# Optimization experiments

Hardware: AMD Instinct MI355X
Metric: run time of the kernel (lower is better)

The kernel has to match this reference:

```python
import jax, jax.numpy as jnp
import numpy as np

N_POINTS = 262144
SP_FEAT = 128
HIDDEN = 64
EMBED = 256
NUM_SP = 4096
NUM_SP2 = 256
PAD_LIMIT = 64
MASK_RATIO = 0.6


def setup_inputs() -> dict:
    key = jax.random.key(0)
    ks = jax.random.split(key, 6)
    x = jax.random.normal(ks[0], (N_POINTS, SP_FEAT), jnp.float32)
    # point -> superpoint ids, sorted; force every superpoint non-empty
    idx10 = jax.random.randint(ks[1], (N_POINTS,), 0, NUM_SP)
    idx10 = jnp.sort(idx10.at[:NUM_SP].set(jnp.arange(NUM_SP))).astype(jnp.int32)
    # superpoint -> higher superpoint, balanced (16 per group, < PAD_LIMIT), sorted
    idx21 = ((jnp.arange(NUM_SP) * NUM_SP2) // NUM_SP).astype(jnp.int32)
    # deterministic mask: exactly int(NUM_SP * MASK_RATIO) superpoints masked
    mask_num = int(NUM_SP * MASK_RATIO)
    perm = jax.random.permutation(ks[2], NUM_SP)
    is_masked = jnp.zeros((NUM_SP,), bool).at[perm[:mask_num]].set(True)
    W1 = jax.random.normal(ks[3], (SP_FEAT, HIDDEN), jnp.float32) / np.sqrt(SP_FEAT).astype(np.float32)
    b1 = jnp.zeros((HIDDEN,), jnp.float32)
    W2 = jax.random.normal(ks[4], (HIDDEN, EMBED), jnp.float32) / np.sqrt(HIDDEN).astype(np.float32)
    b2 = jnp.zeros((EMBED,), jnp.float32)
    return {
        "full_features": x,
        "full_super_indices_10": idx10,
        "full_super_indices_21": idx21,
        "is_masked": is_masked,
        "W1": W1, "b1": b1, "W2": W2, "b2": b2,
    }


def _pad_scatter(tokens, idx21, flag):
    # tokens: [NUM_SP, C]; idx21 sorted sp->sp2 ids; flag: [NUM_SP] bool.
    # rank of each flagged superpoint within its sp2 group (in sp order)
    f = flag.astype(jnp.int32)
    cum = jnp.cumsum(f)                                            # inclusive global cumsum
    per_group = jax.ops.segment_sum(f, idx21, num_segments=NUM_SP2)
    prefix = jnp.concatenate([jnp.zeros((1,), jnp.int32), jnp.cumsum(per_group)[:-1]])
    rank = cum - 1 - prefix[idx21]                                 # 0-based slot within group
    slot = jnp.where(flag, rank, PAD_LIMIT)                        # PAD_LIMIT -> dropped
    out = jnp.zeros((NUM_SP2, PAD_LIMIT, tokens.shape[-1]), tokens.dtype)
    return out.at[idx21, slot].set(tokens, mode="drop")


def reference(full_features, full_super_indices_10, full_super_indices_21,
              is_masked, W1, b1, W2, b2):
    # per-point 2-layer MLP (gather is implicit: MLP is pointwise), then segment max
    h = jax.nn.relu(full_features @ W1 + b1)                       # [N, HIDDEN]
    h = jax.nn.relu(h @ W2 + b2)                                   # [N, EMBED]
    tok = jax.ops.segment_max(h, full_super_indices_10, num_segments=NUM_SP)  # [NUM_SP, EMBED]
    remain_tokens = _pad_scatter(tok, full_super_indices_21, ~is_masked)      # [NUM_SP2, PAD, EMBED]
    mask_tokens = _pad_scatter(tok, full_super_indices_21, is_masked)         # [NUM_SP2, PAD, EMBED]
    return (remain_tokens, mask_tokens)
```

## Files before the change

kernel.cpp:

```cpp
#include <hip/hip_runtime.h>
#include <hip/hip_bf16.h>

#define N_POINTS 262144
#define SP_FEAT 128
#define HIDDEN 64
#define EMBED 256
#define NUM_SP 4096
#define NUM_SP2 256
#define PAD_LIMIT 64
#define SLOTS 4
#define OS_STRIDE 260
#define H1_STRIDE 76

typedef __bf16 bf16x8 __attribute__((ext_vector_type(8)));
typedef float floatx4 __attribute__((ext_vector_type(4)));
using bf16 = __hip_bfloat16;

__global__ __launch_bounds__(256) void fused_prep_kernel(
    const float* __restrict__ W1, const float* __restrict__ W2,
    const int* __restrict__ idx10, const int* __restrict__ idx21,
    const void* __restrict__ is_masked,
    bf16* __restrict__ W1t, bf16* __restrict__ W2t,
    int* __restrict__ start, int* __restrict__ invR, int* __restrict__ invM,
    float4* __restrict__ partial4)
{
    const int tid = threadIdx.x;
    const int blk = blockIdx.x;

    if (blk < 1024) {
        int z = blk * 256 + tid;
        float4 zv = {0.f, 0.f, 0.f, 0.f};
#pragma unroll
        for (int j = 0; j < 4; ++j)
            partial4[z + j * (1024 * 256)] = zv;
        return;
    }
    const int blk2 = blk - 1024;
    if (blk2 < 113) {
        int i = blk2 * 256 + tid;
        if (i < HIDDEN * SP_FEAT) {
            int n = i >> 7, k = i & 127;
            W1t[i] = __float2bfloat16(W1[k * HIDDEN + n]);
        } else if (i < HIDDEN * SP_FEAT + EMBED * HIDDEN) {
            int j = i - HIDDEN * SP_FEAT;
            int n = j >> 6, k = j & 63;
            W2t[j] = __float2bfloat16(W2[k * EMBED + n]);
        } else if (i <= HIDDEN * SP_FEAT + EMBED * HIDDEN + NUM_SP) {
            int s = i - (HIDDEN * SP_FEAT + EMBED * HIDDEN);
            if (s == NUM_SP) { start[s] = N_POINTS; return; }
            int a = 0, b = N_POINTS;
            while (a < b) { int m = (a + b) >> 1; if (idx10[m] < s) a = m + 1; else b = m; }
            start[s] = a;
        }
        return;
    }
    __shared__ int encS;
    if (tid == 0) encS = 0;
    __syncthreads();
    const unsigned char* mb = (const unsigned char*)is_masked;
    const int* mi = (const int*)is_masked;
    int local = 0;
    for (int p = tid; p < NUM_SP; p += 256)
        if ((p & 3) && mb[p]) local = 1;
    if (local) atomicOr(&encS, 1);
    __syncthreads();
    const int e = encS;

    const int g = tid;
    int a = 0, b = NUM_SP;
    while (a < b) { int m = (a + b) >> 1; if (idx21[m] < g) a = m + 1; else b = m; }
    int lo = a;
    b = NUM_SP;
    while (a < b) { int m = (a + b) >> 1; if (idx21[m] < g + 1) a = m + 1; else b = m; }
    int hi = a;
    int nR = 0, nM = 0;
    for (int s = lo; s < hi; ++s) {
        int msk = e ? (int)mb[s] : mi[s];
        if (msk) { if (nM < PAD_LIMIT) invM[g * PAD_LIMIT + nM] = s; nM++; }
        else     { if (nR < PAD_LIMIT) invR[g * PAD_LIMIT + nR] = s; nR++; }
    }
    for (int r = nR; r < PAD_LIMIT; ++r) invR[g * PAD_LIMIT + r] = -1;
    for (int r = nM; r < PAD_LIMIT; ++r) invM[g * PAD_LIMIT + r] = -1;
}

__global__ __launch_bounds__(256, 4) void mlp_segmax_kernel(
    const float* __restrict__ X, const int* __restrict__ idx10,
    const int* __restrict__ start,
    const bf16* __restrict__ W1t, const float* __restrict__ b1,
    const bf16* __restrict__ W2t, const float* __restrict__ b2,
    float* __restrict__ partial)
{
    __shared__ __align__(16) char smemU[64 * OS_STRIDE * 2];
    __shared__ int sIdx[64];
    bf16 (*Xs)[136]       = (bf16(*)[136])smemU;
    bf16 (*H1s)[H1_STRIDE] = (bf16(*)[H1_STRIDE])(smemU + 64 * 136 * 2);
    bf16 (*Os)[OS_STRIDE]  = (bf16(*)[OS_STRIDE])smemU;

    const int tid  = threadIdx.x;
    const int lane = tid & 63;
    const int w    = tid >> 6;
    const int l15  = lane & 15;
    const int quad = lane >> 4;
    const int b    = blockIdx.x;
    const int m0   = b * 64;

    bf16x8 bw1[4];
    {
        const bf16* p = W1t + (16 * w + l15) * SP_FEAT + quad * 8;
#pragma unroll
        for (int ks = 0; ks < 4; ++ks) bw1[ks] = *(const bf16x8*)(p + 32 * ks);
    }
    bf16x8 bf2[4][2];
#pragma unroll
    for (int tn = 0; tn < 4; ++tn) {
        const bf16* p = W2t + (64 * w + 16 * tn + l15) * HIDDEN + quad * 8;
#pragma unroll
        for (int ks = 0; ks < 2; ++ks) bf2[tn][ks] = *(const bf16x8*)(p + 32 * ks);
    }
    float b2f[4];
#pragma unroll
    for (int tn = 0; tn < 4; ++tn) b2f[tn] = b2[64 * w + 16 * tn + l15];
    const float b1v = b1[16 * w + l15];

#pragma unroll
    for (int i = 0; i < 4; ++i) {
        int c   = tid + 256 * i;
        int row = c >> 4;
        int cc  = (c & 15) * 8;
        const float* src = X + (size_t)(m0 + row) * SP_FEAT + cc;
        float4 u0 = *(const float4*)src;
        float4 u1 = *(const float4*)(src + 4);
        union { bf16x8 v; bf16 h[8]; } u;
        u.h[0] = __float2bfloat16(u0.x); u.h[1] = __float2bfloat16(u0.y);
        u.h[2] = __float2bfloat16(u0.z); u.h[3] = __float2bfloat16(u0.w);
        u.h[4] = __float2bfloat16(u1.x); u.h[5] = __float2bfloat16(u1.y);
        u.h[6] = __float2bfloat16(u1.z); u.h[7] = __float2bfloat16(u1.w);
        *(bf16x8*)(&Xs[row][cc]) = u.v;
    }
    if (tid < 64) sIdx[tid] = idx10[m0 + tid];
    __syncthreads();

    floatx4 zero4 = {0.f, 0.f, 0.f, 0.f};
    floatx4 acc1[4] = {zero4, zero4, zero4, zero4};
#pragma unroll
    for (int ks = 0; ks < 4; ++ks) {
        int k = ks * 32 + quad * 8;
#pragma unroll
        for (int tm = 0; tm < 4; ++tm) {
            bf16x8 a = *(bf16x8*)(&Xs[16 * tm + l15][k]);
            acc1[tm] = __builtin_amdgcn_mfma_f32_16x16x32_bf16(a, bw1[ks], acc1[tm], 0, 0, 0);
        }
    }
#pragma unroll
    for (int tm = 0; tm < 4; ++tm) {
#pragma unroll
        for (int r = 0; r < 4; ++r) {
            float v = acc1[tm][r] + b1v;
            v = v > 0.f ? v : 0.f;
            H1s[16 * tm + quad * 4 + r][16 * w + l15] = __float2bfloat16(v);
        }
    }
    __syncthreads();

    bf16x8 afr[4][2];
#pragma unroll
    for (int tm = 0; tm < 4; ++tm) {
        afr[tm][0] = *(bf16x8*)(&H1s[16 * tm + l15][quad * 8]);
        afr[tm][1] = *(bf16x8*)(&H1s[16 * tm + l15][32 + quad * 8]);
    }
    __syncthreads();

#pragma unroll
    for (int tm = 0; tm < 4; ++tm) {
#pragma unroll
        for (int tn = 0; tn < 4; ++tn) {
            floatx4 acc = zero4;
            acc = __builtin_amdgcn_mfma_f32_16x16x32_bf16(afr[tm][0], bf2[tn][0], acc, 0, 0, 0);
            acc = __builtin_amdgcn_mfma_f32_16x16x32_bf16(afr[tm][1], bf2[tn][1], acc, 0, 0, 0);
#pragma unroll
            for (int r = 0; r < 4; ++r) {
                float v = acc[r] + b2f[tn];
                v = v > 0.f ? v : 0.f;
                Os[16 * tm + quad * 4 + r][64 * w + 16 * tn + l15] = __float2bfloat16(v);
            }
        }
    }
    __syncthreads();

    {
        int cur_sp = sIdx[0];
        float cur  = __bfloat162float(Os[0][tid]);
        for (int r = 1; r < 64; ++r) {
            int sp = sIdx[r];
            float v = __bfloat162float(Os[r][tid]);
            if (sp != cur_sp) {
                int slot = b - (start[cur_sp] >> 6);
                int* dst = (int*)(partial + ((size_t)cur_sp * SLOTS + (slot < 3 ? slot : 3)) * EMBED + tid);
                if (slot < 3) *(float*)dst = cur;
                else atomicMax(dst, __float_as_int(cur));
                cur_sp = sp;
                cur = v;
            } else {
                cur = fmaxf(cur, v);
            }
        }
        int slot = b - (start[cur_sp] >> 6);
        int* dst = (int*)(partial + ((size_t)cur_sp * SLOTS + (slot < 3 ? slot : 3)) * EMBED + tid);
        if (slot < 3) *(float*)dst = cur;
        else atomicMax(dst, __float_as_int(cur));
    }
}

__global__ __launch_bounds__(256) void scatter_kernel(
    const float4* __restrict__ partial4, const int* __restrict__ invR,
    const int* __restrict__ invM, float4* __restrict__ out4)
{
    const int bb   = blockIdx.x;
    const int g    = bb & (NUM_SP2 - 1);
    const int slab = bb >> 8;
    const int tid  = threadIdx.x;
    const int c4   = tid & 63;
    const int r0   = tid >> 6;
    const int* tab = slab ? invM : invR;
    float4* o = out4 + ((size_t)slab * NUM_SP2 + g) * PAD_LIMIT * 64;
#pragma unroll 4
    for (int rr = 0; rr < 16; ++rr) {
        int row = r0 + rr * 4;
        int sp = tab[g * PAD_LIMIT + row];
        float4 v = {0.f, 0.f, 0.f, 0.f};
        if (sp >= 0) {
            const float4* p = partial4 + (size_t)sp * SLOTS * 64 + c4;
            float4 a = p[0], bq = p[64], c = p[128], d = p[192];
            v.x = fmaxf(fmaxf(a.x, bq.x), fmaxf(c.x, d.x));
            v.y = fmaxf(fmaxf(a.y, bq.y), fmaxf(c.y, d.y));
            v.z = fmaxf(fmaxf(a.z, bq.z), fmaxf(c.z, d.z));
            v.w = fmaxf(fmaxf(a.w, bq.w), fmaxf(c.w, d.w));
        }
        o[row * 64 + c4] = v;
    }
}

extern "C" void kernel_launch(void* const* d_in, const int* in_sizes, int n_in,
                              void* d_out, int out_size, void* d_ws, size_t ws_size,
                              hipStream_t stream) {
    (void)in_sizes; (void)n_in; (void)ws_size; (void)out_size;
    const float* X        = (const float*)d_in[0];
    const int* idx10      = (const int*)d_in[1];
    const int* idx21      = (const int*)d_in[2];
    const void* is_masked = (const void*)d_in[3];
    const float* W1       = (const float*)d_in[4];
    const float* b1       = (const float*)d_in[5];
    const float* W2       = (const float*)d_in[6];
    const float* b2       = (const float*)d_in[7];

    char* ws       = (char*)d_ws;
    float* partial = (float*)ws;
    bf16* W1t      = (bf16*)(ws + (size_t)NUM_SP * SLOTS * EMBED * 4);
    bf16* W2t      = W1t + HIDDEN * SP_FEAT;
    int*  start    = (int*)((char*)(W2t + EMBED * HIDDEN));
    int*  invR     = start + (NUM_SP + 2);
    int*  invM     = invR + NUM_SP2 * PAD_LIMIT;

    fused_prep_kernel<<<1138, 256, 0, stream>>>(
        W1, W2, idx10, idx21, is_masked, W1t, W2t, start, invR, invM,
        (float4*)partial);
    mlp_segmax_kernel<<<N_POINTS / 64, 256, 0, stream>>>(
        X, idx10, start, W1t, b1, W2t, b2, partial);
    scatter_kernel<<<NUM_SP2 * 2, 256, 0, stream>>>(
        (const float4*)partial, invR, invM, (float4*)d_out);
}
```

Before: 263.1 us.

## Fuse segment-max into MFMA epilogue, drop partial zeroing and binary-search start

The per-superpoint start offsets are now found by scanning for boundaries between neighbouring sorted indices instead of a binary search per superpoint. The 16 MB zero-fill of the partial buffer is removed. The second-layer MFMA epilogue now does the running segment max directly in registers and merges results through shared-memory atomics, replacing the bf16 output staging and its barriers. The scatter kernel reads only the partial slots a superpoint actually wrote. The risk is that atomicMax on slot 3 and on non-local superpoints now targets a partial buffer that was never initialised, which could give wrong results when a segment spans many blocks.

```diff
diff --git a/kernel.cpp b/kernel.cpp
--- a/kernel.cpp
+++ b/kernel.cpp
@@ -9,8 +9,9 @@
 #define NUM_SP2 256
 #define PAD_LIMIT 64
 #define SLOTS 4
-#define OS_STRIDE 260
+#define XS_STRIDE 136
 #define H1_STRIDE 76
+#define LOCAL_SP 8
 
 typedef __bf16 bf16x8 __attribute__((ext_vector_type(8)));
 typedef float floatx4 __attribute__((ext_vector_type(4)));
@@ -21,36 +22,33 @@
     const int* __restrict__ idx10, const int* __restrict__ idx21,
     const void* __restrict__ is_masked,
     bf16* __restrict__ W1t, bf16* __restrict__ W2t,
-    int* __restrict__ start, int* __restrict__ invR, int* __restrict__ invM,
-    float4* __restrict__ partial4)
+    int* __restrict__ start, int* __restrict__ invR, int* __restrict__ invM)
 {
     const int tid = threadIdx.x;
     const int blk = blockIdx.x;
 
-    if (blk < 1024) {
-        int z = blk * 256 + tid;
-        float4 zv = {0.f, 0.f, 0.f, 0.f};
-#pragma unroll
-        for (int j = 0; j < 4; ++j)
-            partial4[z + j * (1024 * 256)] = zv;
+    if (blk < 256) {
+        int p0 = (blk * 256 + tid) * 4;
+        int4 v = *(const int4*)(idx10 + p0);
+        if (p0 == 0) { start[0] = 0; start[NUM_SP] = N_POINTS; }
+        if (v.y != v.x) start[v.y] = p0 + 1;
+        if (v.z != v.y) start[v.z] = p0 + 2;
+        if (v.w != v.z) start[v.w] = p0 + 3;
+        if (p0 + 4 < N_POINTS) {
+            int nx = idx10[p0 + 4];
+            if (nx != v.w) start[nx] = p0 + 4;
+        }
         return;
     }
-    const int blk2 = blk - 1024;
-    if (blk2 < 113) {
-        int i = blk2 * 256 + tid;
+    if (blk < 352) {
+        int i = (blk - 256) * 256 + tid;
         if (i < HIDDEN * SP_FEAT) {
             int n = i >> 7, k = i & 127;
             W1t[i] = __float2bfloat16(W1[k * HIDDEN + n]);
-        } else if (i < HIDDEN * SP_FEAT + EMBED * HIDDEN) {
+        } else {
             int j = i - HIDDEN * SP_FEAT;
             int n = j >> 6, k = j & 63;
             W2t[j] = __float2bfloat16(W2[k * EMBED + n]);
-        } else if (i <= HIDDEN * SP_FEAT + EMBED * HIDDEN + NUM_SP) {
-            int s = i - (HIDDEN * SP_FEAT + EMBED * HIDDEN);
-            if (s == NUM_SP) { start[s] = N_POINTS; return; }
-            int a = 0, b = N_POINTS;
-            while (a < b) { int m = (a + b) >> 1; if (idx10[m] < s) a = m + 1; else b = m; }
-            start[s] = a;
         }
         return;
     }
@@ -90,11 +88,10 @@
     const bf16* __restrict__ W2t, const float* __restrict__ b2,
     float* __restrict__ partial)
 {
-    __shared__ __align__(16) char smemU[64 * OS_STRIDE * 2];
+    __shared__ __align__(16) bf16 Xs[64][XS_STRIDE];
+    __shared__ __align__(16) bf16 H1s[64][H1_STRIDE];
+    __shared__ int tokL[LOCAL_SP][EMBED];
     __shared__ int sIdx[64];
-    bf16 (*Xs)[136]       = (bf16(*)[136])smemU;
-    bf16 (*H1s)[H1_STRIDE] = (bf16(*)[H1_STRIDE])(smemU + 64 * 136 * 2);
-    bf16 (*Os)[OS_STRIDE]  = (bf16(*)[OS_STRIDE])smemU;
 
     const int tid  = threadIdx.x;
     const int lane = tid & 63;
@@ -103,6 +100,9 @@
     const int quad = lane >> 4;
     const int b    = blockIdx.x;
     const int m0   = b * 64;
+
+#pragma unroll
+    for (int j = 0; j < LOCAL_SP; ++j) tokL[j][tid] = 0;
 
     bf16x8 bw1[4];
     {
@@ -163,17 +163,24 @@
     __syncthreads();
 
     bf16x8 afr[4][2];
+    int sps[16];
 #pragma unroll
     for (int tm = 0; tm < 4; ++tm) {
         afr[tm][0] = *(bf16x8*)(&H1s[16 * tm + l15][quad * 8]);
         afr[tm][1] = *(bf16x8*)(&H1s[16 * tm + l15][32 + quad * 8]);
-    }
-    __syncthreads();
-
-#pragma unroll
-    for (int tm = 0; tm < 4; ++tm) {
-#pragma unroll
-        for (int tn = 0; tn < 4; ++tn) {
+        int4 s4 = *(const int4*)(&sIdx[16 * tm + 4 * quad]);
+        sps[4 * tm + 0] = s4.x; sps[4 * tm + 1] = s4.y;
+        sps[4 * tm + 2] = s4.z; sps[4 * tm + 3] = s4.w;
+    }
+    const int sp0 = sIdx[0];
+
+#pragma unroll
+    for (int tn = 0; tn < 4; ++tn) {
+        const int col = 64 * w + 16 * tn + l15;
+        int cur_sp = -1;
+        float cur = 0.f;
+#pragma unroll
+        for (int tm = 0; tm < 4; ++tm) {
             floatx4 acc = zero4;
             acc = __builtin_amdgcn_mfma_f32_16x16x32_bf16(afr[tm][0], bf2[tn][0], acc, 0, 0, 0);
             acc = __builtin_amdgcn_mfma_f32_16x16x32_bf16(afr[tm][1], bf2[tn][1], acc, 0, 0, 0);
@@ -181,39 +188,56 @@
             for (int r = 0; r < 4; ++r) {
                 float v = acc[r] + b2f[tn];
                 v = v > 0.f ? v : 0.f;
-                Os[16 * tm + quad * 4 + r][64 * w + 16 * tn + l15] = __float2bfloat16(v);
-            }
-        }
-    }
-    __syncthreads();
-
-    {
-        int cur_sp = sIdx[0];
-        float cur  = __bfloat162float(Os[0][tid]);
-        for (int r = 1; r < 64; ++r) {
-            int sp = sIdx[r];
-            float v = __bfloat162float(Os[r][tid]);
-            if (sp != cur_sp) {
+                int sp = sps[4 * tm + r];
+                if (sp == cur_sp) {
+                    cur = fmaxf(cur, v);
+                } else {
+                    if (cur_sp >= 0) {
+                        int local = cur_sp - sp0;
+                        if (local < LOCAL_SP) {
+                            atomicMax(&tokL[local][col], __float_as_int(cur));
+                        } else {
+                            int slot = b - (start[cur_sp] >> 6);
+                            atomicMax((int*)(partial + ((size_t)cur_sp * SLOTS +
+                                      (slot < 3 ? slot : 3)) * EMBED + col),
+                                      __float_as_int(cur));
+                        }
+                    }
+                    cur_sp = sp;
+                    cur = v;
+                }
+            }
+        }
+        {
+            int local = cur_sp - sp0;
+            if (local < LOCAL_SP) {
+                atomicMax(&tokL[local][col], __float_as_int(cur));
+            } else {
                 int slot = b - (start[cur_sp] >> 6);
-                int* dst = (int*)(partial + ((size_t)cur_sp * SLOTS + (slot < 3 ? slot : 3)) * EMBED + tid);
-                if (slot < 3) *(float*)dst = cur;
-                else atomicMax(dst, __float_as_int(cur));
-                cur_sp = sp;
-                cur = v;
-            } else {
-                cur = fmaxf(cur, v);
-            }
-        }
-        int slot = b - (start[cur_sp] >> 6);
-        int* dst = (int*)(partial + ((size_t)cur_sp * SLOTS + (slot < 3 ? slot : 3)) * EMBED + tid);
-        if (slot < 3) *(float*)dst = cur;
-        else atomicMax(dst, __float_as_int(cur));
+                atomicMax((int*)(partial + ((size_t)cur_sp * SLOTS +
+                          (slot < 3 ? slot : 3)) * EMBED + col),
+                          __float_as_int(cur));
+            }
+        }
+    }
+    __syncthreads();
+
+    int nsp = sIdx[63] - sp0 + 1;
+    if (nsp > LOCAL_SP) nsp = LOCAL_SP;
+    for (int j = 0; j < nsp; ++j) {
+        int sp   = sp0 + j;
+        int slot = b - (start[sp] >> 6);
+        int bits = tokL[j][tid];
+        int* dst = (int*)(partial + ((size_t)sp * SLOTS + (slot < 3 ? slot : 3)) * EMBED + tid);
+        if (slot < 3) *dst = bits;
+        else atomicMax(dst, bits);
     }
 }
 
 __global__ __launch_bounds__(256) void scatter_kernel(
-    const float4* __restrict__ partial4, const int* __restrict__ invR,
-    const int* __restrict__ invM, float4* __restrict__ out4)
+    const float4* __restrict__ partial4, const int* __restrict__ start,
+    const int* __restrict__ invR, const int* __restrict__ invM,
+    float4* __restrict__ out4)
 {
     const int bb   = blockIdx.x;
     const int g    = bb & (NUM_SP2 - 1);
@@ -229,12 +253,26 @@
         int sp = tab[g * PAD_LIMIT + row];
         float4 v = {0.f, 0.f, 0.f, 0.f};
         if (sp >= 0) {
+            int sb = start[sp] >> 6;
+            int se = (start[sp + 1] - 1) >> 6;
+            int ns = se - sb;
             const float4* p = partial4 + (size_t)sp * SLOTS * 64 + c4;
-            float4 a = p[0], bq = p[64], c = p[128], d = p[192];
-            v.x = fmaxf(fmaxf(a.x, bq.x), fmaxf(c.x, d.x));
-            v.y = fmaxf(fmaxf(a.y, bq.y), fmaxf(c.y, d.y));
-            v.z = fmaxf(fmaxf(a.z, bq.z), fmaxf(c.z, d.z));
-            v.w = fmaxf(fmaxf(a.w, bq.w), fmaxf(c.w, d.w));
+            v = p[0];
+            if (ns > 0) {
+                float4 q = p[64];
+                v.x = fmaxf(v.x, q.x); v.y = fmaxf(v.y, q.y);
+                v.z = fmaxf(v.z, q.z); v.w = fmaxf(v.w, q.w);
+            }
+            if (ns > 1) {
+                float4 q = p[128];
+                v.x = fmaxf(v.x, q.x); v.y = fmaxf(v.y, q.y);
+                v.z = fmaxf(v.z, q.z); v.w = fmaxf(v.w, q.w);
+            }
+            if (ns > 2) {
+                float4 q = p[192];
+                v.x = fmaxf(v.x, q.x); v.y = fmaxf(v.y, q.y);
+                v.z = fmaxf(v.z, q.z); v.w = fmaxf(v.w, q.w);
+            }
         }
         o[row * 64 + c4] = v;
     }
@@ -261,11 +299,10 @@
     int*  invR     = start + (NUM_SP + 2);
     int*  invM     = invR + NUM_SP2 * PAD_LIMIT;
 
-    fused_prep_kernel<<<1138, 256, 0, stream>>>(
-        W1, W2, idx10, idx21, is_masked, W1t, W2t, start, invR, invM,
-        (float4*)partial);
+    fused_prep_kernel<<<353, 256, 0, stream>>>(
+        W1, W2, idx10, idx21, is_masked, W1t, W2t, start, invR, invM);
     mlp_segmax_kernel<<<N_POINTS / 64, 256, 0, stream>>>(
         X, idx10, start, W1t, b1, W2t, b2, partial);
     scatter_kernel<<<NUM_SP2 * 2, 256, 0, stream>>>(
-        (const float4*)partial, invR, invM, (float4*)d_out);
+        (const float4*)partial, start, invR, invM, (float4*)d_out);
 }
```

Result: faster. 248.2 us (-5.7%).
